# Performance work log

Measured on AMD Instinct MI355X. Metric: run time of the kernel, lower is better.

The kernel has to match this reference:

```python
import jax, jax.numpy as jnp
import numpy as np

B, S, L, H, D, DF = 2, 1024, 2, 8, 512, 2048
DK = D // H  # head dim (dk == dv == 64)
EPS = 1e-5


def _ln(x, g, b):
    m = jnp.mean(x, axis=-1, keepdims=True)
    v = jnp.mean((x - m) ** 2, axis=-1, keepdims=True)
    return (x - m) / jnp.sqrt(v + EPS) * g + b


def setup_inputs() -> dict:
    key = jax.random.key(0)
    ks = jax.random.split(key, 8)
    sd = 1.0 / np.sqrt(D)
    sf = 1.0 / np.sqrt(DF)
    inp = {
        "src": jax.random.normal(ks[0], (B, S, D), jnp.float32),
        "Wq": jax.random.normal(ks[1], (L, D, D), jnp.float32) * sd,
        "bq": jnp.zeros((L, D), jnp.float32),
        "Wk": jax.random.normal(ks[2], (L, D, D), jnp.float32) * sd,
        "bk": jnp.zeros((L, D), jnp.float32),
        "Wv": jax.random.normal(ks[3], (L, D, D), jnp.float32) * sd,
        "bv": jnp.zeros((L, D), jnp.float32),
        "Wo": jax.random.normal(ks[4], (L, D, D), jnp.float32) * sd,
        "bo": jnp.zeros((L, D), jnp.float32),
        "W1": jax.random.normal(ks[5], (L, D, DF), jnp.float32) * sd,
        "b1": jnp.zeros((L, DF), jnp.float32),
        "W2": jax.random.normal(ks[6], (L, DF, D), jnp.float32) * sf,
        "b2": jnp.zeros((L, D), jnp.float32),
        "g1": jnp.ones((L, D), jnp.float32),
        "be1": jnp.zeros((L, D), jnp.float32),
        "g2": jnp.ones((L, D), jnp.float32),
        "be2": jnp.zeros((L, D), jnp.float32),
        "gf": jnp.ones((D,), jnp.float32),
        "bef": jnp.zeros((D,), jnp.float32),
    }
    return inp


def _heads(x):
    # [B,S,D] -> [B,H,S,DK]
    return x.reshape(B, S, H, DK).transpose(0, 2, 1, 3)


def _causal_linear_attention(q, k, v):
    # Faithful to torch: cumsum of per-step KV outer products, then query contraction.
    kv = jnp.einsum("bhsk,bhsv->bhskv", k, v)      # [B,H,S,DK,DK]
    cum = jnp.cumsum(kv, axis=2)                     # prefix sums over sequence
    return jnp.einsum("bhsk,bhskv->bhsv", q, cum)   # [B,H,S,DK]


def reference(src, Wq, bq, Wk, bk, Wv, bv, Wo, bo, W1, b1, W2, b2,
              g1, be1, g2, be2, gf, bef):
    x = src
    for i in range(L):
        q = _heads(x @ Wq[i] + bq[i])
        k = _heads(x @ Wk[i] + bk[i])
        v = _heads(x @ Wv[i] + bv[i])
        att = _causal_linear_attention(q, k, v)
        att = att.transpose(0, 2, 1, 3).reshape(B, S, D)
        att = att @ Wo[i] + bo[i]
        x = _ln(x + att, g1[i], be1[i])              # post-norm (normalize_before=False)
        ff = jax.nn.relu(x @ W1[i] + b1[i]) @ W2[i] + b2[i]
        x = _ln(x + ff, g2[i], be2[i])
    return _ln(x, gf, bef)                            # final encoder LayerNorm
```

## Files before the change

kernel.cpp:

```cpp
#include <hip/hip_runtime.h>
#include <hip/hip_bf16.h>

#define DEV static __device__ __forceinline__

typedef __attribute__((ext_vector_type(8))) short short8;
typedef __attribute__((ext_vector_type(4))) float f32x4;

DEV unsigned short f2b(float f){
  unsigned int u = __float_as_uint(f);
  return (unsigned short)((u + 0x7FFFu + ((u >> 16) & 1u)) >> 16);
}
DEV float b2f(unsigned short h){ return __uint_as_float(((unsigned int)h) << 16); }
DEV float load_in(const void* p, size_t i, int isbf){
  return isbf ? b2f(((const unsigned short*)p)[i]) : ((const float*)p)[i];
}
DEV void load_lds16(const unsigned short* g, unsigned short* l){
  __builtin_amdgcn_global_load_lds(
      (const __attribute__((address_space(1))) void*)g,
      (__attribute__((address_space(3))) void*)l, 16, 0, 0);
}

DEV int detect_isbf_block(const void* src){
  __shared__ int cnt[4];
  int tid = threadIdx.x;
  float v = b2f(((const unsigned short*)src)[2 * tid]);
  float av = fabsf(v);
  bool sane = ((av < 64.0f) && (av > 9.5e-7f)) || (v == 0.0f);
  unsigned long long m = __ballot(sane);
  if ((tid & 63) == 0) cnt[tid >> 6] = __popcll(m);
  __syncthreads();
  int tot = cnt[0] + cnt[1] + cnt[2] + cnt[3];
  __syncthreads();
  return tot > 128;
}

struct WDesc { const void* src; long src_off; unsigned short* dst; int K; int N; int tstart; };
struct SDesc { const void* src; int src_off; int dstart; };
struct IngestParams {
  WDesc wd[12];
  SDesc sd[22];
  float* sdst; int stotal;
  const void* src;
  float* xf; unsigned short* xb;
};

__global__ __launch_bounds__(256) void ingest_all(IngestParams P){
  __shared__ float tile[32][33];
  int isbf = detect_isbf_block(P.src);
  int b = blockIdx.x, tid = threadIdx.x;
  if (b < 6144){
    int t = 0;
    #pragma unroll
    for (int i = 1; i < 12; ++i) if (b >= P.wd[i].tstart) t = i;
    WDesc d = P.wd[t];
    int r = b - d.tstart;
    int tiles_x = d.N >> 5;
    int tx = r % tiles_x, ty = r / tiles_x;
    int lx = tid & 31, ly = tid >> 5;
    #pragma unroll
    for (int i = 0; i < 4; ++i){
      int row = ty*32 + ly + i*8;
      int col = tx*32 + lx;
      tile[ly + i*8][lx] = load_in(d.src, (size_t)d.src_off + (size_t)row*d.N + col, isbf);
    }
    __syncthreads();
    #pragma unroll
    for (int i = 0; i < 4; ++i){
      int orow = tx*32 + ly + i*8;
      int ocol = ty*32 + lx;
      d.dst[(size_t)orow*d.K + ocol] = f2b(tile[lx][ly + i*8]);
    }
  } else if (b < 10240){
    int i = (b - 6144)*256 + tid;
    float v = load_in(P.src, (size_t)i, isbf);
    P.xf[i] = v; P.xb[i] = f2b(v);
  } else {
    int i = (b - 10240)*256 + tid;
    if (i < P.stotal){
      int t = 0;
      #pragma unroll
      for (int j = 1; j < 22; ++j) if (i >= P.sd[j].dstart) t = j;
      P.sdst[i] = load_in(P.sd[t].src, (size_t)P.sd[t].src_off + (i - P.sd[t].dstart), isbf);
    }
  }
}

struct GemmArgs {
  const unsigned short* A;
  const unsigned short* Bt;
  const float* bias;
  float* Cf;
  unsigned short* Cb;
  int K;
  int lda, ldb, ldc;
  int cshift, cmask;
  size_t cstride;
  size_t cfz;
  int relu;
};

template<int BN>
__global__ __launch_bounds__(256) void gemm_bt(GemmArgs g){
  constexpr int NI = (BN == 128) ? 4 : 2;
  constexpr int NJ = 4;
  __shared__ __align__(16) unsigned short sA[128*32];
  __shared__ __align__(16) unsigned short sB[BN*32];
  int tid = threadIdx.x;
  int koff = blockIdx.z * g.K;
  int K = g.K, lda = g.lda, ldb = g.ldb;
  size_t bm = (size_t)blockIdx.y * 128, bn = (size_t)blockIdx.x * BN;
  int lane = tid & 63, wv = tid >> 6, quad = lane >> 4, l16 = lane & 15;
  int wm = (BN == 128) ? (wv >> 1) * 64 : wv * 32;
  int wn = (BN == 128) ? (wv & 1) * 64 : 0;
  f32x4 acc[NI][NJ];
  #pragma unroll
  for (int i=0;i<NI;++i)
    #pragma unroll
    for (int j=0;j<NJ;++j) acc[i][j] = (f32x4){0.f,0.f,0.f,0.f};
  const unsigned short* Ap = g.A  + (bm + (tid>>2))*lda + koff + (tid&3)*8;
  const unsigned short* Bp = g.Bt + (bn + (tid>>2))*ldb + koff + (tid&3)*8;
  for (int ko = 0; ko < K; ko += 32){
    __syncthreads();
    load_lds16(Ap + ko,                  &sA[tid*8]);
    load_lds16(Ap + (size_t)64*lda + ko, &sA[2048 + tid*8]);
    load_lds16(Bp + ko,                  &sB[tid*8]);
    if (BN == 128)
      load_lds16(Bp + (size_t)64*ldb + ko, &sB[2048 + tid*8]);
    __syncthreads();
    short8 af[NI], bfv[NJ];
    #pragma unroll
    for (int i=0;i<NI;++i) af[i]  = *(const short8*)&sA[(wm + i*16 + l16)*32 + quad*8];
    #pragma unroll
    for (int j=0;j<NJ;++j) bfv[j] = *(const short8*)&sB[(wn + j*16 + l16)*32 + quad*8];
    #pragma unroll
    for (int i=0;i<NI;++i)
      #pragma unroll
      for (int j=0;j<NJ;++j)
        acc[i][j] = __builtin_amdgcn_mfma_f32_16x16x32_bf16(af[i], bfv[j], acc[i][j], 0,0,0);
  }
  float* Cf = g.Cf ? g.Cf + (size_t)blockIdx.z * g.cfz : nullptr;
  unsigned short* Cb = g.Cb;
  #pragma unroll
  for (int j=0;j<NJ;++j){
    int col = (int)bn + wn + j*16 + l16;
    float bv = g.bias ? g.bias[col] : 0.f;
    size_t cbase = ((size_t)(col >> g.cshift))*g.cstride + (col & g.cmask);
    #pragma unroll
    for (int i=0;i<NI;++i){
      #pragma unroll
      for (int r=0;r<4;++r){
        int row = (int)bm + wm + i*16 + quad*4 + r;
        float v = acc[i][j][r] + bv;
        if (g.relu) v = fmaxf(v, 0.f);
        size_t idx = cbase + (size_t)row*g.ldc;
        if (Cf) Cf[idx] = v;
        if (Cb) Cb[idx] = f2b(v);
      }
    }
  }
}

#define ATT_S 1024
#define ATT_D 512

__global__ __launch_bounds__(256) void attn_kernel(
    const unsigned short* q, const unsigned short* k, const unsigned short* v,
    unsigned short* att)
{
  __shared__ __align__(16) unsigned short sQ [64*72];
  __shared__ __align__(16) unsigned short sK [64*72];
  __shared__ __align__(16) unsigned short sVt[64*72];
  __shared__ __align__(16) unsigned short sKt[64*72];
  __shared__ __align__(16) float sKV[64*68];
  int tid = threadIdx.x;
  int c = blockIdx.x, bh = blockIdx.y;
  int b = bh >> 3, h = bh & 7;
  const size_t hoff = ((size_t)b*ATT_S)*ATT_D + h*64;
  int lane = tid & 63, wv = tid >> 6, quad = lane >> 4, l16 = lane & 15;

  f32x4 accS[4];
  #pragma unroll
  for (int j=0;j<4;++j) accS[j] = (f32x4){0.f,0.f,0.f,0.f};
  int t = lane, vc = wv*8;
  for (int cc = 0; cc < c; ++cc){
    const size_t bcc = hoff + (size_t)cc*64*ATT_D;
    const unsigned short* vp = v + bcc + (size_t)t*ATT_D;
    const unsigned short* kp = k + bcc + (size_t)t*ATT_D;
    float4 v0 = *(const float4*)(vp + vc);
    float4 v1 = *(const float4*)(vp + vc + 32);
    float4 k0 = *(const float4*)(kp + vc);
    float4 k1 = *(const float4*)(kp + vc + 32);
    __syncthreads();
    {
      const unsigned short* pv0 = (const unsigned short*)&v0;
      const unsigned short* pv1 = (const unsigned short*)&v1;
      const unsigned short* pk0 = (const unsigned short*)&k0;
      const unsigned short* pk1 = (const unsigned short*)&k1;
      #pragma unroll
      for (int e = 0; e < 8; ++e){
        sVt[(vc+e)*72 + t]    = pv0[e];
        sVt[(vc+32+e)*72 + t] = pv1[e];
        sKt[(vc+e)*72 + t]    = pk0[e];
        sKt[(vc+32+e)*72 + t] = pk1[e];
      }
    }
    __syncthreads();
    #pragma unroll
    for (int kk=0;kk<2;++kk){
      short8 a = *(const short8*)&sVt[(wv*16 + l16)*72 + kk*32 + quad*8];
      #pragma unroll
      for (int j=0;j<4;++j){
        short8 bb = *(const short8*)&sKt[(j*16 + l16)*72 + kk*32 + quad*8];
        accS[j] = __builtin_amdgcn_mfma_f32_16x16x32_bf16(a, bb, accS[j], 0,0,0);
      }
    }
  }
  #pragma unroll
  for (int j=0;j<4;++j)
    #pragma unroll
    for (int rr=0;rr<4;++rr)
      sKV[(wv*16 + quad*4 + rr)*68 + j*16 + l16] = accS[j][rr];

  const size_t base = hoff + (size_t)c*64*ATT_D;
  int r = tid >> 2, c8 = (tid & 3)*8;
  const unsigned short* qp = q + base + (size_t)r*ATT_D;
  const unsigned short* kp = k + base + (size_t)r*ATT_D;
  float4 q0 = *(const float4*)(qp + c8);
  float4 q1 = *(const float4*)(qp + c8 + 32);
  float4 k0 = *(const float4*)(kp + c8);
  float4 k1 = *(const float4*)(kp + c8 + 32);
  const unsigned short* vp = v + base + (size_t)t*ATT_D;
  float4 v0 = *(const float4*)(vp + vc);
  float4 v1 = *(const float4*)(vp + vc + 32);
  __syncthreads();
  *(float4*)&sQ[r*72 + c8]      = q0;
  *(float4*)&sQ[r*72 + c8 + 32] = q1;
  *(float4*)&sK[r*72 + c8]      = k0;
  *(float4*)&sK[r*72 + c8 + 32] = k1;
  {
    const unsigned short* pv0 = (const unsigned short*)&v0;
    const unsigned short* pv1 = (const unsigned short*)&v1;
    #pragma unroll
    for (int e=0;e<8;++e){
      sVt[(vc+e)*72 + t]    = pv0[e];
      sVt[(vc+32+e)*72 + t] = pv1[e];
    }
  }
  __syncthreads();

  f32x4 accQ[4];
  #pragma unroll
  for (int j=0;j<4;++j) accQ[j] = (f32x4){0.f,0.f,0.f,0.f};
  #pragma unroll
  for (int kk=0;kk<2;++kk){
    short8 a = *(const short8*)&sQ[(wv*16 + l16)*72 + kk*32 + quad*8];
    #pragma unroll
    for (int j=0;j<4;++j){
      short8 bb = *(const short8*)&sK[(j*16 + l16)*72 + kk*32 + quad*8];
      accQ[j] = __builtin_amdgcn_mfma_f32_16x16x32_bf16(a, bb, accQ[j], 0,0,0);
    }
  }
  __syncthreads();

  #pragma unroll
  for (int j=0;j<4;++j)
    #pragma unroll
    for (int rr=0;rr<4;++rr){
      int i  = wv*16 + quad*4 + rr;
      int cj = j*16 + l16;
      sK[i*72 + cj] = f2b((i >= cj) ? accQ[j][rr] : 0.f);
    }

  f32x4 accO[4];
  #pragma unroll
  for (int j=0;j<4;++j) accO[j] = (f32x4){0.f,0.f,0.f,0.f};
  #pragma unroll
  for (int kk=0;kk<2;++kk){
    short8 a = *(const short8*)&sQ[(wv*16 + l16)*72 + kk*32 + quad*8];
    #pragma unroll
    for (int j=0;j<4;++j){
      const float* pf = &sKV[(j*16 + l16)*68 + kk*32 + quad*8];
      short8 bb;
      #pragma unroll
      for (int e=0;e<8;++e) ((unsigned short*)&bb)[e] = f2b(pf[e]);
      accO[j] = __builtin_amdgcn_mfma_f32_16x16x32_bf16(a, bb, accO[j], 0,0,0);
    }
  }
  __syncthreads();

  #pragma unroll
  for (int kk=0;kk<2;++kk){
    short8 a = *(const short8*)&sK[(wv*16 + l16)*72 + kk*32 + quad*8];
    #pragma unroll
    for (int j=0;j<4;++j){
      short8 bb = *(const short8*)&sVt[(j*16 + l16)*72 + kk*32 + quad*8];
      accO[j] = __builtin_amdgcn_mfma_f32_16x16x32_bf16(a, bb, accO[j], 0,0,0);
    }
  }
  #pragma unroll
  for (int j=0;j<4;++j)
    #pragma unroll
    for (int rr=0;rr<4;++rr){
      int i  = wv*16 + quad*4 + rr;
      int cj = j*16 + l16;
      att[base + (size_t)i*ATT_D + cj] = f2b(accO[j][rr]);
    }
}

__global__ __launch_bounds__(256) void add_ln_kernel(
    const float* x, const float* p, int np, const float* bias,
    const float* g, const float* bta,
    float* outf, unsigned short* outb, void* outd, const void* dsrc, int rows)
{
  int isbf = 0;
  if (dsrc) isbf = detect_isbf_block(dsrc);
  int row = blockIdx.x*4 + (threadIdx.x >> 6);
  int lane = threadIdx.x & 63;
  if (row >= rows) return;
  const float* xr = x + (size_t)row*512;
  float a[8];
  *(float4*)&a[0] = *(const float4*)(xr + lane*4);
  *(float4*)&a[4] = *(const float4*)(xr + 256 + lane*4);
  for (int s = 0; s < np; ++s){
    const float* pr = p + (size_t)s*1048576 + (size_t)row*512;
    float yb[8];
    *(float4*)&yb[0] = *(const float4*)(pr + lane*4);
    *(float4*)&yb[4] = *(const float4*)(pr + 256 + lane*4);
    #pragma unroll
    for (int e=0;e<8;++e) a[e] += yb[e];
  }
  if (bias){
    float bb2[8];
    *(float4*)&bb2[0] = *(const float4*)(bias + lane*4);
    *(float4*)&bb2[4] = *(const float4*)(bias + 256 + lane*4);
    #pragma unroll
    for (int e=0;e<8;++e) a[e] += bb2[e];
  }
  float s = 0.f, qq = 0.f;
  #pragma unroll
  for (int e=0;e<8;++e){ s += a[e]; qq += a[e]*a[e]; }
  #pragma unroll
  for (int off=32; off>0; off>>=1){
    s  += __shfl_xor(s,  off, 64);
    qq += __shfl_xor(qq, off, 64);
  }
  float mean = s * (1.f/512.f);
  float var  = qq * (1.f/512.f) - mean*mean;
  float rstd = rsqrtf(var + 1e-5f);
  float gg[8], bb[8];
  *(float4*)&gg[0] = *(const float4*)(g + lane*4);
  *(float4*)&gg[4] = *(const float4*)(g + 256 + lane*4);
  *(float4*)&bb[0] = *(const float4*)(bta + lane*4);
  *(float4*)&bb[4] = *(const float4*)(bta + 256 + lane*4);
  #pragma unroll
  for (int e=0;e<8;++e) a[e] = (a[e]-mean)*rstd*gg[e] + bb[e];
  if (outf){
    float* orow = outf + (size_t)row*512;
    *(float4*)(orow + lane*4)       = *(float4*)&a[0];
    *(float4*)(orow + 256 + lane*4) = *(float4*)&a[4];
  }
  if (outb){
    unsigned short* orow = outb + (size_t)row*512;
    #pragma unroll
    for (int e=0;e<4;++e){ orow[lane*4+e] = f2b(a[e]); orow[256+lane*4+e] = f2b(a[4+e]); }
  }
  if (outd){
    if (isbf){
      unsigned short* od = (unsigned short*)outd + (size_t)row*512;
      #pragma unroll
      for (int e=0;e<4;++e){ od[lane*4+e] = f2b(a[e]); od[256+lane*4+e] = f2b(a[4+e]); }
    } else {
      float* od = (float*)outd + (size_t)row*512;
      *(float4*)(od + lane*4)       = *(float4*)&a[0];
      *(float4*)(od + 256 + lane*4) = *(float4*)&a[4];
    }
  }
}

extern "C" void kernel_launch(void* const* d_in, const int* in_sizes, int n_in,
                              void* d_out, int out_size, void* d_ws, size_t ws_size,
                              hipStream_t stream)
{
  (void)in_sizes; (void)n_in; (void)out_size; (void)ws_size;
  const void* src = d_in[0];
  const void* Wq = d_in[1];  const void* bq = d_in[2];
  const void* Wk = d_in[3];  const void* bk = d_in[4];
  const void* Wv = d_in[5];  const void* bv = d_in[6];
  const void* Wo = d_in[7];  const void* bo = d_in[8];
  const void* W1 = d_in[9];  const void* b1 = d_in[10];
  const void* W2 = d_in[11]; const void* b2 = d_in[12];
  const void* g1 = d_in[13]; const void* be1 = d_in[14];
  const void* g2 = d_in[15]; const void* be2 = d_in[16];
  const void* gf = d_in[17]; const void* bef = d_in[18];

  char* W = (char*)d_ws;
  float* smalls          = (float*)(W + 256);
  unsigned short* wt     = (unsigned short*)(W + 65536);
  float* x_f             = (float*)(W + 12648448);
  unsigned short* x_b    = (unsigned short*)(W + 16842752);
  unsigned short* q_b    = (unsigned short*)(W + 18939904);
  unsigned short* att_b  = (unsigned short*)(W + 25231360);
  float* pp              = (float*)(W + 27328512);
  unsigned short* h1_b   = (unsigned short*)(W + 44105728);
  unsigned short* k_b = q_b + 1048576;
  unsigned short* v_b = q_b + 2097152;

  IngestParams ip;
  {
    const void* wsrc[6] = {Wq, Wk, Wv, Wo, W1, W2};
    int wK[6] = {512,512,512,512,512,2048};
    int wN[6] = {512,512,512,512,2048,512};
    long wsz[6] = {262144,262144,262144,262144,1048576,1048576};
    int tstart = 0; size_t dsto = 0;
    for (int l=0;l<2;++l)
      for (int ti=0;ti<6;++ti){
        int idx = l*6+ti;
        ip.wd[idx].src = wsrc[ti];
        ip.wd[idx].src_off = (long)l * wsz[ti];
        ip.wd[idx].dst = wt + dsto;
        ip.wd[idx].K = wK[ti]; ip.wd[idx].N = wN[ti];
        ip.wd[idx].tstart = tstart;
        tstart += (wK[ti]/32)*(wN[ti]/32);
        dsto += (size_t)wsz[ti];
      }
    const void* ss[10] = {bq,bk,bv,bo,b1,b2,g1,be1,g2,be2};
    int slen[10] = {512,512,512,512,2048,512,512,512,512,512};
    int dcur = 0, di = 0;
    for (int l=0;l<2;++l)
      for (int ti=0;ti<10;++ti){
        ip.sd[di].src = ss[ti];
        ip.sd[di].src_off = l * slen[ti];
        ip.sd[di].dstart = dcur;
        dcur += slen[ti]; ++di;
      }
    ip.sd[20].src = gf;  ip.sd[20].src_off = 0; ip.sd[20].dstart = dcur; dcur += 512;
    ip.sd[21].src = bef; ip.sd[21].src_off = 0; ip.sd[21].dstart = dcur; dcur += 512;
    ip.sdst = smalls; ip.stotal = dcur;
    ip.src = src; ip.xf = x_f; ip.xb = x_b;
    ingest_all<<<dim3(10296), 256, 0, stream>>>(ip);
  }

  for (int l = 0; l < 2; ++l){
    unsigned short* WqkvT = wt + (size_t)l*3145728;
    unsigned short* WoT   = WqkvT + 786432;
    unsigned short* W1T   = WqkvT + 1048576;
    unsigned short* W2T   = WqkvT + 2097152;
    float* base  = smalls + l*6656;
    float* p_bqkv= base;
    float* p_bo  = base + 1536;
    float* p_b1  = base + 2048;
    float* p_b2  = base + 4096;
    float* p_g1  = base + 4608;
    float* p_be1 = base + 5120;
    float* p_g2  = base + 5632;
    float* p_be2 = base + 6144;

    GemmArgs qkv = {};
    qkv.A = x_b; qkv.Bt = WqkvT; qkv.bias = p_bqkv;
    qkv.Cf = nullptr; qkv.Cb = q_b;
    qkv.K = 512; qkv.lda = 512; qkv.ldb = 512; qkv.ldc = 512;
    qkv.cshift = 9; qkv.cmask = 511; qkv.cstride = 1048576; qkv.cfz = 0; qkv.relu = 0;
    gemm_bt<64><<<dim3(24,16,1), 256, 0, stream>>>(qkv);

    attn_kernel<<<dim3(16,16), 256, 0, stream>>>(q_b, k_b, v_b, att_b);

    GemmArgs go = {};
    go.A = att_b; go.Bt = WoT; go.bias = nullptr;
    go.Cf = pp; go.Cb = nullptr;
    go.K = 256; go.lda = 512; go.ldb = 512; go.ldc = 512;
    go.cshift = 30; go.cmask = 0x3fffffff; go.cstride = 0; go.cfz = 1048576; go.relu = 0;
    gemm_bt<64><<<dim3(8,16,2), 256, 0, stream>>>(go);

    add_ln_kernel<<<dim3(512), 256, 0, stream>>>(x_f, pp, 2, p_bo, p_g1, p_be1,
                                                 x_f, x_b, nullptr, nullptr, 2048);

    GemmArgs f1 = {};
    f1.A = x_b; f1.Bt = W1T; f1.bias = p_b1;
    f1.Cf = nullptr; f1.Cb = h1_b;
    f1.K = 512; f1.lda = 512; f1.ldb = 512; f1.ldc = 2048;
    f1.cshift = 30; f1.cmask = 0x3fffffff; f1.cstride = 0; f1.cfz = 0; f1.relu = 1;
    gemm_bt<128><<<dim3(16,16,1), 256, 0, stream>>>(f1);

    GemmArgs f2 = {};
    f2.A = h1_b; f2.Bt = W2T; f2.bias = nullptr;
    f2.Cf = pp; f2.Cb = nullptr;
    f2.K = 512; f2.lda = 2048; f2.ldb = 2048; f2.ldc = 512;
    f2.cshift = 30; f2.cmask = 0x3fffffff; f2.cstride = 0; f2.cfz = 1048576; f2.relu = 0;
    gemm_bt<64><<<dim3(8,16,4), 256, 0, stream>>>(f2);

    add_ln_kernel<<<dim3(512), 256, 0, stream>>>(x_f, pp, 4, p_b2, p_g2, p_be2,
                                                 x_f, x_b, nullptr, nullptr, 2048);
  }

  add_ln_kernel<<<dim3(512), 256, 0, stream>>>(x_f, nullptr, 0, nullptr,
                                               smalls + 13312, smalls + 13824,
                                               nullptr, nullptr, d_out, src, 2048);
}
```

Before: 289.7 us.

## Split linear attention into parallel chunk-state and output kernels; unify GEMM tiles to 128x128

The attention kernel used to recompute every earlier chunk's K^T V product serially inside each block. It is now split in two. One kernel computes each chunk's 64x64 KV state in parallel and writes it to a float workspace. A second kernel prefix-sums the earlier states from global memory and then does the intra-chunk work. Separately, the GEMM is fixed at 128x128 tiles, so the QKV, Wo and FFN2 launches use half as many blocks. This adds a kernel launch and global traffic for the states, and the larger tiles reduce parallelism on small grids.

```diff
diff --git a/kernel.cpp b/kernel.cpp
--- a/kernel.cpp
+++ b/kernel.cpp
@@ -99,24 +99,20 @@
   int relu;
 };
 
-template<int BN>
 __global__ __launch_bounds__(256) void gemm_bt(GemmArgs g){
-  constexpr int NI = (BN == 128) ? 4 : 2;
-  constexpr int NJ = 4;
   __shared__ __align__(16) unsigned short sA[128*32];
-  __shared__ __align__(16) unsigned short sB[BN*32];
+  __shared__ __align__(16) unsigned short sB[128*32];
   int tid = threadIdx.x;
   int koff = blockIdx.z * g.K;
   int K = g.K, lda = g.lda, ldb = g.ldb;
-  size_t bm = (size_t)blockIdx.y * 128, bn = (size_t)blockIdx.x * BN;
+  size_t bm = (size_t)blockIdx.y * 128, bn = (size_t)blockIdx.x * 128;
   int lane = tid & 63, wv = tid >> 6, quad = lane >> 4, l16 = lane & 15;
-  int wm = (BN == 128) ? (wv >> 1) * 64 : wv * 32;
-  int wn = (BN == 128) ? (wv & 1) * 64 : 0;
-  f32x4 acc[NI][NJ];
-  #pragma unroll
-  for (int i=0;i<NI;++i)
-    #pragma unroll
-    for (int j=0;j<NJ;++j) acc[i][j] = (f32x4){0.f,0.f,0.f,0.f};
+  int wm = (wv >> 1) * 64, wn = (wv & 1) * 64;
+  f32x4 acc[4][4];
+  #pragma unroll
+  for (int i=0;i<4;++i)
+    #pragma unroll
+    for (int j=0;j<4;++j) acc[i][j] = (f32x4){0.f,0.f,0.f,0.f};
   const unsigned short* Ap = g.A  + (bm + (tid>>2))*lda + koff + (tid&3)*8;
   const unsigned short* Bp = g.Bt + (bn + (tid>>2))*ldb + koff + (tid&3)*8;
   for (int ko = 0; ko < K; ko += 32){
@@ -124,29 +120,28 @@
     load_lds16(Ap + ko,                  &sA[tid*8]);
     load_lds16(Ap + (size_t)64*lda + ko, &sA[2048 + tid*8]);
     load_lds16(Bp + ko,                  &sB[tid*8]);
-    if (BN == 128)
-      load_lds16(Bp + (size_t)64*ldb + ko, &sB[2048 + tid*8]);
+    load_lds16(Bp + (size_t)64*ldb + ko, &sB[2048 + tid*8]);
     __syncthreads();
-    short8 af[NI], bfv[NJ];
-    #pragma unroll
-    for (int i=0;i<NI;++i) af[i]  = *(const short8*)&sA[(wm + i*16 + l16)*32 + quad*8];
-    #pragma unroll
-    for (int j=0;j<NJ;++j) bfv[j] = *(const short8*)&sB[(wn + j*16 + l16)*32 + quad*8];
-    #pragma unroll
-    for (int i=0;i<NI;++i)
+    short8 af[4], bfv[4];
+    #pragma unroll
+    for (int i=0;i<4;++i) af[i]  = *(const short8*)&sA[(wm + i*16 + l16)*32 + quad*8];
+    #pragma unroll
+    for (int j=0;j<4;++j) bfv[j] = *(const short8*)&sB[(wn + j*16 + l16)*32 + quad*8];
+    #pragma unroll
+    for (int i=0;i<4;++i)
       #pragma unroll
-      for (int j=0;j<NJ;++j)
+      for (int j=0;j<4;++j)
         acc[i][j] = __builtin_amdgcn_mfma_f32_16x16x32_bf16(af[i], bfv[j], acc[i][j], 0,0,0);
   }
   float* Cf = g.Cf ? g.Cf + (size_t)blockIdx.z * g.cfz : nullptr;
   unsigned short* Cb = g.Cb;
   #pragma unroll
-  for (int j=0;j<NJ;++j){
+  for (int j=0;j<4;++j){
     int col = (int)bn + wn + j*16 + l16;
     float bv = g.bias ? g.bias[col] : 0.f;
     size_t cbase = ((size_t)(col >> g.cshift))*g.cstride + (col & g.cmask);
     #pragma unroll
-    for (int i=0;i<NI;++i){
+    for (int i=0;i<4;++i){
       #pragma unroll
       for (int r=0;r<4;++r){
         int row = (int)bm + wm + i*16 + quad*4 + r;
@@ -163,65 +158,92 @@
 #define ATT_S 1024
 #define ATT_D 512
 
-__global__ __launch_bounds__(256) void attn_kernel(
+__global__ __launch_bounds__(256) void attn_state_kernel(
+    const unsigned short* k, const unsigned short* v, float* states)
+{
+  __shared__ __align__(16) unsigned short sVt[64*72];
+  __shared__ __align__(16) unsigned short sKt[64*72];
+  int tid = threadIdx.x;
+  int c = blockIdx.x, bh = blockIdx.y;
+  int b = bh >> 3, h = bh & 7;
+  const size_t base = ((size_t)b*ATT_S + (size_t)c*64)*ATT_D + h*64;
+  int lane = tid & 63, wv = tid >> 6, quad = lane >> 4, l16 = lane & 15;
+
+  int t = lane, vc = wv*8;
+  const unsigned short* vp = v + base + (size_t)t*ATT_D;
+  const unsigned short* kp = k + base + (size_t)t*ATT_D;
+  float4 v0 = *(const float4*)(vp + vc);
+  float4 v1 = *(const float4*)(vp + vc + 32);
+  float4 k0 = *(const float4*)(kp + vc);
+  float4 k1 = *(const float4*)(kp + vc + 32);
+  {
+    const unsigned short* pv0 = (const unsigned short*)&v0;
+    const unsigned short* pv1 = (const unsigned short*)&v1;
+    const unsigned short* pk0 = (const unsigned short*)&k0;
+    const unsigned short* pk1 = (const unsigned short*)&k1;
+    #pragma unroll
+    for (int e = 0; e < 8; ++e){
+      sVt[(vc+e)*72 + t]    = pv0[e];
+      sVt[(vc+32+e)*72 + t] = pv1[e];
+      sKt[(vc+e)*72 + t]    = pk0[e];
+      sKt[(vc+32+e)*72 + t] = pk1[e];
+    }
+  }
+  __syncthreads();
+
+  f32x4 acc[4];
+  #pragma unroll
+  for (int j=0;j<4;++j) acc[j] = (f32x4){0.f,0.f,0.f,0.f};
+  #pragma unroll
+  for (int kk=0;kk<2;++kk){
+    short8 a = *(const short8*)&sVt[(wv*16 + l16)*72 + kk*32 + quad*8];
+    #pragma unroll
+    for (int j=0;j<4;++j){
+      short8 bb = *(const short8*)&sKt[(j*16 + l16)*72 + kk*32 + quad*8];
+      acc[j] = __builtin_amdgcn_mfma_f32_16x16x32_bf16(a, bb, acc[j], 0,0,0);
+    }
+  }
+  float* st = states + ((size_t)bh*16 + c)*4096;
+  #pragma unroll
+  for (int j=0;j<4;++j)
+    #pragma unroll
+    for (int rr=0;rr<4;++rr)
+      st[(wv*16 + quad*4 + rr)*64 + j*16 + l16] = acc[j][rr];
+}
+
+__global__ __launch_bounds__(256) void attn_out_kernel(
     const unsigned short* q, const unsigned short* k, const unsigned short* v,
-    unsigned short* att)
+    const float* states, unsigned short* att)
 {
   __shared__ __align__(16) unsigned short sQ [64*72];
   __shared__ __align__(16) unsigned short sK [64*72];
   __shared__ __align__(16) unsigned short sVt[64*72];
-  __shared__ __align__(16) unsigned short sKt[64*72];
   __shared__ __align__(16) float sKV[64*68];
   int tid = threadIdx.x;
   int c = blockIdx.x, bh = blockIdx.y;
   int b = bh >> 3, h = bh & 7;
-  const size_t hoff = ((size_t)b*ATT_S)*ATT_D + h*64;
+  const size_t base = ((size_t)b*ATT_S + (size_t)c*64)*ATT_D + h*64;
   int lane = tid & 63, wv = tid >> 6, quad = lane >> 4, l16 = lane & 15;
 
-  f32x4 accS[4];
-  #pragma unroll
-  for (int j=0;j<4;++j) accS[j] = (f32x4){0.f,0.f,0.f,0.f};
-  int t = lane, vc = wv*8;
+  float4 racc[4];
+  #pragma unroll
+  for (int u=0;u<4;++u) racc[u] = (float4){0.f,0.f,0.f,0.f};
+  const float* sbase = states + (size_t)bh*16*4096;
   for (int cc = 0; cc < c; ++cc){
-    const size_t bcc = hoff + (size_t)cc*64*ATT_D;
-    const unsigned short* vp = v + bcc + (size_t)t*ATT_D;
-    const unsigned short* kp = k + bcc + (size_t)t*ATT_D;
-    float4 v0 = *(const float4*)(vp + vc);
-    float4 v1 = *(const float4*)(vp + vc + 32);
-    float4 k0 = *(const float4*)(kp + vc);
-    float4 k1 = *(const float4*)(kp + vc + 32);
-    __syncthreads();
-    {
-      const unsigned short* pv0 = (const unsigned short*)&v0;
-      const unsigned short* pv1 = (const unsigned short*)&v1;
-      const unsigned short* pk0 = (const unsigned short*)&k0;
-      const unsigned short* pk1 = (const unsigned short*)&k1;
-      #pragma unroll
-      for (int e = 0; e < 8; ++e){
-        sVt[(vc+e)*72 + t]    = pv0[e];
-        sVt[(vc+32+e)*72 + t] = pv1[e];
-        sKt[(vc+e)*72 + t]    = pk0[e];
-        sKt[(vc+32+e)*72 + t] = pk1[e];
-      }
-    }
-    __syncthreads();
-    #pragma unroll
-    for (int kk=0;kk<2;++kk){
-      short8 a = *(const short8*)&sVt[(wv*16 + l16)*72 + kk*32 + quad*8];
-      #pragma unroll
-      for (int j=0;j<4;++j){
-        short8 bb = *(const short8*)&sKt[(j*16 + l16)*72 + kk*32 + quad*8];
-        accS[j] = __builtin_amdgcn_mfma_f32_16x16x32_bf16(a, bb, accS[j], 0,0,0);
-      }
-    }
-  }
-  #pragma unroll
-  for (int j=0;j<4;++j)
-    #pragma unroll
-    for (int rr=0;rr<4;++rr)
-      sKV[(wv*16 + quad*4 + rr)*68 + j*16 + l16] = accS[j][rr];
-
-  const size_t base = hoff + (size_t)c*64*ATT_D;
+    const float4* sp = (const float4*)(sbase + (size_t)cc*4096);
+    #pragma unroll
+    for (int u=0;u<4;++u){
+      float4 t4 = sp[tid + u*256];
+      racc[u].x += t4.x; racc[u].y += t4.y; racc[u].z += t4.z; racc[u].w += t4.w;
+    }
+  }
+  #pragma unroll
+  for (int u=0;u<4;++u){
+    int e = (tid + u*256)*4;
+    int row = e >> 6, col = e & 63;
+    *(float4*)&sKV[row*68 + col] = racc[u];
+  }
+
   int r = tid >> 2, c8 = (tid & 3)*8;
   const unsigned short* qp = q + base + (size_t)r*ATT_D;
   const unsigned short* kp = k + base + (size_t)r*ATT_D;
@@ -229,10 +251,10 @@
   float4 q1 = *(const float4*)(qp + c8 + 32);
   float4 k0 = *(const float4*)(kp + c8);
   float4 k1 = *(const float4*)(kp + c8 + 32);
+  int t = lane, vc = wv*8;
   const unsigned short* vp = v + base + (size_t)t*ATT_D;
   float4 v0 = *(const float4*)(vp + vc);
   float4 v1 = *(const float4*)(vp + vc + 32);
-  __syncthreads();
   *(float4*)&sQ[r*72 + c8]      = q0;
   *(float4*)&sQ[r*72 + c8 + 32] = q1;
   *(float4*)&sK[r*72 + c8]      = k0;
@@ -248,16 +270,16 @@
   }
   __syncthreads();
 
-  f32x4 accQ[4];
-  #pragma unroll
-  for (int j=0;j<4;++j) accQ[j] = (f32x4){0.f,0.f,0.f,0.f};
+  f32x4 accS[4];
+  #pragma unroll
+  for (int j=0;j<4;++j) accS[j] = (f32x4){0.f,0.f,0.f,0.f};
   #pragma unroll
   for (int kk=0;kk<2;++kk){
     short8 a = *(const short8*)&sQ[(wv*16 + l16)*72 + kk*32 + quad*8];
     #pragma unroll
     for (int j=0;j<4;++j){
       short8 bb = *(const short8*)&sK[(j*16 + l16)*72 + kk*32 + quad*8];
-      accQ[j] = __builtin_amdgcn_mfma_f32_16x16x32_bf16(a, bb, accQ[j], 0,0,0);
+      accS[j] = __builtin_amdgcn_mfma_f32_16x16x32_bf16(a, bb, accS[j], 0,0,0);
     }
   }
   __syncthreads();
@@ -268,7 +290,7 @@
     for (int rr=0;rr<4;++rr){
       int i  = wv*16 + quad*4 + rr;
       int cj = j*16 + l16;
-      sK[i*72 + cj] = f2b((i >= cj) ? accQ[j][rr] : 0.f);
+      sK[i*72 + cj] = f2b((i >= cj) ? accS[j][rr] : 0.f);
     }
 
   f32x4 accO[4];
@@ -402,6 +424,7 @@
   unsigned short* att_b  = (unsigned short*)(W + 25231360);
   float* pp              = (float*)(W + 27328512);
   unsigned short* h1_b   = (unsigned short*)(W + 44105728);
+  float* states          = (float*)(W + 52494336);
   unsigned short* k_b = q_b + 1048576;
   unsigned short* v_b = q_b + 2097152;
 
@@ -460,16 +483,17 @@
     qkv.Cf = nullptr; qkv.Cb = q_b;
     qkv.K = 512; qkv.lda = 512; qkv.ldb = 512; qkv.ldc = 512;
     qkv.cshift = 9; qkv.cmask = 511; qkv.cstride = 1048576; qkv.cfz = 0; qkv.relu = 0;
-    gemm_bt<64><<<dim3(24,16,1), 256, 0, stream>>>(qkv);
-
-    attn_kernel<<<dim3(16,16), 256, 0, stream>>>(q_b, k_b, v_b, att_b);
+    gemm_bt<<<dim3(12,16,1), 256, 0, stream>>>(qkv);
+
+    attn_state_kernel<<<dim3(16,16), 256, 0, stream>>>(k_b, v_b, states);
+    attn_out_kernel<<<dim3(16,16), 256, 0, stream>>>(q_b, k_b, v_b, states, att_b);
 
     GemmArgs go = {};
     go.A = att_b; go.Bt = WoT; go.bias = nullptr;
     go.Cf = pp; go.Cb = nullptr;
     go.K = 256; go.lda = 512; go.ldb = 512; go.ldc = 512;
     go.cshift = 30; go.cmask = 0x3fffffff; go.cstride = 0; go.cfz = 1048576; go.relu = 0;
-    gemm_bt<64><<<dim3(8,16,2), 256, 0, stream>>>(go);
+    gemm_bt<<<dim3(4,16,2), 256, 0, stream>>>(go);
 
     add_ln_kernel<<<dim3(512), 256, 0, stream>>>(x_f, pp, 2, p_bo, p_g1, p_be1,
                                                  x_f, x_b, nullptr, nullptr, 2048);
@@ -479,14 +503,14 @@
     f1.Cf = nullptr; f1.Cb = h1_b;
     f1.K = 512; f1.lda = 512; f1.ldb = 512; f1.ldc = 2048;
     f1.cshift = 30; f1.cmask = 0x3fffffff; f1.cstride = 0; f1.cfz = 0; f1.relu = 1;
-    gemm_bt<128><<<dim3(16,16,1), 256, 0, stream>>>(f1);
+    gemm_bt<<<dim3(16,16,1), 256, 0, stream>>>(f1);
 
     GemmArgs f2 = {};
     f2.A = h1_b; f2.Bt = W2T; f2.bias = nullptr;
     f2.Cf = pp; f2.Cb = nullptr;
     f2.K = 512; f2.lda = 2048; f2.ldb = 2048; f2.ldc = 512;
     f2.cshift = 30; f2.cmask = 0x3fffffff; f2.cstride = 0; f2.cfz = 1048576; f2.relu = 0;
-    gemm_bt<64><<<dim3(8,16,4), 256, 0, stream>>>(f2);
+    gemm_bt<<<dim3(4,16,4), 256, 0, stream>>>(f2);
 
     add_ln_kernel<<<dim3(512), 256, 0, stream>>>(x_f, pp, 4, p_b2, p_g2, p_be2,
                                                  x_f, x_b, nullptr, nullptr, 2048);
```

Result: no change. 295.3 us (+1.9%).
